# Performance work log

Hardware: AMD Instinct MI355X
Metric: run time of the kernel (lower is better)

The kernel has to match this reference:

```python
import jax, jax.numpy as jnp
import numpy as np

H = 16          # num heads
DH = 64         # head dim
D = H * DH      # hidden = 1024


def setup_inputs() -> dict:
    key = jax.random.key(0)
    ks = jax.random.split(key, 9)
    s = 1.0 / np.sqrt(D)
    return {
        "hidden_states": jax.random.normal(ks[0], (4, 2048, D), dtype=jnp.float32),
        "Wq": jax.random.normal(ks[1], (D, D), dtype=jnp.float32) * s,
        "bq": jax.random.normal(ks[2], (D,), dtype=jnp.float32) * 0.02,
        "Wk": jax.random.normal(ks[3], (D, D), dtype=jnp.float32) * s,
        "bk": jax.random.normal(ks[4], (D,), dtype=jnp.float32) * 0.02,
        "Wv": jax.random.normal(ks[5], (D, D), dtype=jnp.float32) * s,
        "bv": jax.random.normal(ks[6], (D,), dtype=jnp.float32) * 0.02,
        "Wo": jax.random.normal(ks[7], (D, D), dtype=jnp.float32) * s,
        "bo": jax.random.normal(ks[8], (D,), dtype=jnp.float32) * 0.02,
    }


def _split_heads(x):  # [B,S,D] -> [B,H,S,DH]
    B, S, _ = x.shape
    return x.reshape(B, S, H, DH).transpose(0, 2, 1, 3)


def reference(hidden_states, Wq, bq, Wk, bk, Wv, bv, Wo, bo):
    # torch Linear: y = x @ W.T + b  (W stored as [out, in])
    q = _split_heads(jnp.einsum('bsd,ed->bse', hidden_states, Wq) + bq)
    k = _split_heads(jnp.einsum('bsd,ed->bse', hidden_states, Wk) + bk)
    v = _split_heads(jnp.einsum('bsd,ed->bse', hidden_states, Wv) + bv)
    scores = jnp.einsum('bhqd,bhkd->bhqk', q, k) / np.sqrt(DH)
    probs = jax.nn.softmax(scores, axis=-1)  # fused softmax+matmul in original
    ctx = jnp.einsum('bhqk,bhkd->bhqd', probs, v)
    B, _, S, _ = ctx.shape
    ctx = ctx.transpose(0, 2, 1, 3).reshape(B, S, D)
    out = jnp.einsum('bsd,ed->bse', ctx, Wo) + bo
    return out  # weights are None (vis=False); dropout rate asserted 0
```

## Files before the change

### kernel.cpp

```cpp
#include <hip/hip_runtime.h>


typedef __bf16 bf16;
typedef __bf16 bf16x8 __attribute__((ext_vector_type(8)));
typedef __bf16 bf16x4 __attribute__((ext_vector_type(4)));
typedef float  floatx4 __attribute__((ext_vector_type(4)));

#define NB   4
#define SEQ  2048
#define NH   16
#define DH   64
#define DIM  1024
#define MTOT (NB * SEQ)

#define CEXP 0.18033688f

__device__ __forceinline__ floatx4 zero4() {
    floatx4 z; z[0] = 0.f; z[1] = 0.f; z[2] = 0.f; z[3] = 0.f; return z;
}

__device__ __forceinline__ void load_lds16(const bf16* g, bf16* l) {
    __builtin_amdgcn_global_load_lds(
        (__attribute__((address_space(1))) void*)g,
        (__attribute__((address_space(3))) void*)l,
        16, 0, 0);
}

__global__ __launch_bounds__(256) void cvt_all(const float* __restrict__ X,
                                               const float* __restrict__ w0,
                                               const float* __restrict__ w1,
                                               const float* __restrict__ w2,
                                               const float* __restrict__ w3,
                                               bf16* __restrict__ Xb,
                                               bf16* __restrict__ Wb) {
    const size_t MD = (size_t)MTOT * DIM;
    const size_t DD = (size_t)DIM * DIM;
    size_t i = ((size_t)blockIdx.x * 256 + threadIdx.x) * 4;
    float4 f; bf16* dst;
    if (i < MD) {
        f = *(const float4*)(X + i);
        dst = Xb + i;
    } else {
        size_t off = i - MD;
        int w = (int)(off >> 20);
        size_t wi = off & (DD - 1);
        const float* ws = (w == 0) ? w0 : (w == 1) ? w1 : (w == 2) ? w2 : w3;
        f = *(const float4*)(ws + wi);
        dst = Wb + off;
    }
    bf16x4 o;
    o[0] = (bf16)f.x; o[1] = (bf16)f.y; o[2] = (bf16)f.z; o[3] = (bf16)f.w;
    *(bf16x4*)dst = o;
}

#define QKV_TILE(T_, DO_STAGE_, WAITSTR_) do {                                 \
    const bf16* bA_ = smem + ((T_) & 3) * 16384;                               \
    const bf16* bB_ = bA_ + 8192;                                              \
    if (DO_STAGE_) {                                                           \
        bf16* sA_ = smem + (((T_) + 3) & 3) * 16384;                           \
        const int ko_ = ((T_) + 3) * 32;                                       \
        load_lds16(gA0 + ko_, sA_ + soff0);                                    \
        load_lds16(gA1 + ko_, sA_ + soff1);                                    \
        load_lds16(gB0 + ko_, sA_ + 8192 + soff0);                             \
        load_lds16(gB1 + ko_, sA_ + 8192 + soff1);                             \
    }                                                                          \
    bf16x8 afr_[4], bfg_[4];                                                   \
    _Pragma("unroll")                                                          \
    for (int mf = 0; mf < 4; mf++) afr_[mf] = *(const bf16x8*)(bA_ + aoff[mf]);\
    _Pragma("unroll")                                                          \
    for (int nf = 0; nf < 4; nf++) bfg_[nf] = *(const bf16x8*)(bB_ + boff[nf]);\
    __builtin_amdgcn_s_setprio(1);                                             \
    _Pragma("unroll")                                                          \
    for (int mf = 0; mf < 4; mf++)                                             \
        _Pragma("unroll")                                                      \
        for (int nf = 0; nf < 4; nf++)                                         \
            acc[mf][nf] = __builtin_amdgcn_mfma_f32_16x16x32_bf16(             \
                afr_[mf], bfg_[nf], acc[mf][nf], 0, 0, 0);                     \
    __builtin_amdgcn_s_setprio(0);                                             \
    _Pragma("unroll")                                                          \
    for (int mf = 0; mf < 4; mf++)                                             \
        afr_[mf] = *(const bf16x8*)(bA_ + aoff[4 + mf]);                       \
    __builtin_amdgcn_s_setprio(1);                                             \
    _Pragma("unroll")                                                          \
    for (int mf = 0; mf < 4; mf++)                                             \
        _Pragma("unroll")                                                      \
        for (int nf = 0; nf < 4; nf++)                                         \
            acc[4 + mf][nf] = __builtin_amdgcn_mfma_f32_16x16x32_bf16(         \
                afr_[mf], bfg_[nf], acc[4 + mf][nf], 0, 0, 0);                 \
    __builtin_amdgcn_s_setprio(0);                                             \
    asm volatile(WAITSTR_ ::: "memory");                                       \
    __builtin_amdgcn_s_barrier();                                              \
} while (0)

__global__ __launch_bounds__(512, 2) void gemm_qkv(const bf16* __restrict__ A,
                                                   const bf16* __restrict__ W,
                                                   const float* __restrict__ bq,
                                                   const float* __restrict__ bk,
                                                   const float* __restrict__ bv,
                                                   bf16* __restrict__ Qo,
                                                   bf16* __restrict__ Ko,
                                                   bf16* __restrict__ Vt) {
    __shared__ __align__(16) bf16 smem[4 * 16384];

    const int tid  = threadIdx.x;
    const int wave = tid >> 6, lane = tid & 63;
    const int quad = lane >> 4, l16 = lane & 15;
    const int wr = wave >> 2, wc = wave & 3;

    const int wg = (blockIdx.x & 7) * 48 + (blockIdx.x >> 3);
    const int mt = wg / 12, inner = wg % 12;
    const int sel = inner >> 2, nt = inner & 3;
    const int m0 = mt * 256, n0 = nt * 256;

    const bf16* Wsel = W + (size_t)(sel * DIM + n0) * DIM;
    const float* bias = (sel == 0) ? bq : (sel == 1) ? bk : bv;

    int aoff[8], boff[4];
#pragma unroll
    for (int mf = 0; mf < 8; mf++) {
        const int row = wr * 128 + mf * 16 + l16;
        aoff[mf] = row * 32 + ((quad ^ ((row >> 1) & 3)) * 8);
    }
#pragma unroll
    for (int nf = 0; nf < 4; nf++) {
        const int row = wc * 64 + nf * 16 + l16;
        boff[nf] = row * 32 + ((quad ^ ((row >> 1) & 3)) * 8);
    }

    const int c0 = tid, c1 = tid + 512;
    const int ra0 = c0 >> 2, qa0 = (c0 & 3) ^ ((ra0 >> 1) & 3);
    const int ra1 = c1 >> 2, qa1 = (c1 & 3) ^ ((ra1 >> 1) & 3);
    const bf16* gA0 = A + (size_t)(m0 + ra0) * DIM + qa0 * 8;
    const bf16* gA1 = A + (size_t)(m0 + ra1) * DIM + qa1 * 8;
    const bf16* gB0 = Wsel + (size_t)ra0 * DIM + qa0 * 8;
    const bf16* gB1 = Wsel + (size_t)ra1 * DIM + qa1 * 8;
    const int soff0 = (wave * 64) * 8;
    const int soff1 = (512 + wave * 64) * 8;

    floatx4 acc[8][4];
#pragma unroll
    for (int mf = 0; mf < 8; mf++)
#pragma unroll
        for (int nf = 0; nf < 4; nf++) acc[mf][nf] = zero4();

#pragma unroll
    for (int kt = 0; kt < 3; kt++) {
        bf16* sA = smem + kt * 16384;
        bf16* sB = sA + 8192;
        load_lds16(gA0 + kt * 32, sA + soff0);
        load_lds16(gA1 + kt * 32, sA + soff1);
        load_lds16(gB0 + kt * 32, sB + soff0);
        load_lds16(gB1 + kt * 32, sB + soff1);
    }
    asm volatile("s_waitcnt vmcnt(8)" ::: "memory");
    __builtin_amdgcn_s_barrier();

    const int NT = DIM / 32;
#pragma unroll 1
    for (int t = 0; t < NT - 3; t++)
        QKV_TILE(t, true, "s_waitcnt vmcnt(8)");
    QKV_TILE(NT - 3, false, "s_waitcnt vmcnt(4)");
    QKV_TILE(NT - 2, false, "s_waitcnt vmcnt(0)");
    QKV_TILE(NT - 1, false, "s_waitcnt vmcnt(0)");

    if (sel < 2) {
        bf16* C = (sel == 0) ? Qo : Ko;
        const float scale = (sel == 0) ? CEXP : 1.0f;
#pragma unroll
        for (int mf = 0; mf < 8; mf++) {
            const int rbase = m0 + wr * 128 + mf * 16 + quad * 4;
#pragma unroll
            for (int nf = 0; nf < 4; nf++) {
                const int col = n0 + wc * 64 + nf * 16 + l16;
                const float bval = bias[col];
#pragma unroll
                for (int i = 0; i < 4; i++)
                    C[(size_t)(rbase + i) * DIM + col] =
                        (bf16)((acc[mf][nf][i] + bval) * scale);
            }
        }
    } else {
        const int b  = m0 >> 11;
        const int s0 = m0 & (SEQ - 1);
#pragma unroll
        for (int mf = 0; mf < 8; mf++) {
            const int mb = wr * 128 + mf * 16 + quad * 4;
#pragma unroll
            for (int nf = 0; nf < 4; nf++) {
                const int n_loc = wc * 64 + nf * 16 + l16;
                const float bval = bias[n0 + n_loc];
                bf16x4 pk;
#pragma unroll
                for (int i = 0; i < 4; i++) pk[i] = (bf16)(acc[mf][nf][i] + bval);
                const int e = n_loc * 256 + (((mb * 2) ^ ((n_loc & 7) << 4)) >> 1);
                *(bf16x4*)(smem + e) = pk;
            }
        }
        asm volatile("s_waitcnt lgkmcnt(0)" ::: "memory");
        __builtin_amdgcn_s_barrier();
#pragma unroll
        for (int p = 0; p < 16; p++) {
            const int c = p * 512 + tid;
            const int n_loc = c >> 5, mc = (c & 31) * 8;
            const int e = n_loc * 256 + (((mc * 2) ^ ((n_loc & 7) << 4)) >> 1);
            bf16x8 v = *(const bf16x8*)(smem + e);
            const int dg = n0 + n_loc;
            const int hh = dg >> 6, d = dg & 63;
            bf16* op = Vt + ((size_t)(b * NH + hh) * DH + d) * SEQ + s0 + mc;
            *(bf16x8*)op = v;
        }
    }
}

__global__ __launch_bounds__(256) void gemm_out(const bf16* __restrict__ A,
                                                const bf16* __restrict__ W,
                                                const float* __restrict__ bias,
                                                float* __restrict__ C) {
    __shared__ __align__(16) bf16 As[128 * 32];
    __shared__ __align__(16) bf16 Bs[128 * 32];

    const int tid  = threadIdx.x;
    const int wave = tid >> 6, lane = tid & 63;
    const int quad = lane >> 4, l16 = lane & 15;
    const int m0 = blockIdx.y * 128, n0 = blockIdx.x * 128;
    const int wm = (wave & 1) * 64, wn = (wave >> 1) * 64;

    floatx4 acc[4][4];
#pragma unroll
    for (int mi = 0; mi < 4; mi++)
#pragma unroll
        for (int ni = 0; ni < 4; ni++) acc[mi][ni] = zero4();

    for (int k0 = 0; k0 < DIM; k0 += 32) {
        __syncthreads();
#pragma unroll
        for (int i = 0; i < 2; i++) {
            const int cb = wave * 128 + i * 64;
            const int c  = cb + lane;
            const int row = c >> 2;
            const int kc  = (c & 3) * 8;
            load_lds16(A + (size_t)(m0 + row) * DIM + k0 + kc, &As[cb * 8]);
            load_lds16(W + (size_t)(n0 + row) * DIM + k0 + kc, &Bs[cb * 8]);
        }
        __syncthreads();

        bf16x8 af[4], bfr[4];
#pragma unroll
        for (int mi = 0; mi < 4; mi++)
            af[mi] = *(const bf16x8*)&As[(wm + mi * 16 + l16) * 32 + quad * 8];
#pragma unroll
        for (int ni = 0; ni < 4; ni++)
            bfr[ni] = *(const bf16x8*)&Bs[(wn + ni * 16 + l16) * 32 + quad * 8];
#pragma unroll
        for (int mi = 0; mi < 4; mi++)
#pragma unroll
            for (int ni = 0; ni < 4; ni++)
                acc[mi][ni] = __builtin_amdgcn_mfma_f32_16x16x32_bf16(
                    af[mi], bfr[ni], acc[mi][ni], 0, 0, 0);
    }

#pragma unroll
    for (int mi = 0; mi < 4; mi++) {
        const int rbase = m0 + wm + mi * 16 + quad * 4;
#pragma unroll
        for (int ni = 0; ni < 4; ni++) {
            const int col = n0 + wn + ni * 16 + l16;
            const float bval = bias[col];
#pragma unroll
            for (int i = 0; i < 4; i++)
                C[(size_t)(rbase + i) * DIM + col] = acc[mi][ni][i] + bval;
        }
    }
}

__global__ __launch_bounds__(256, 2) void attn_kernel(const bf16* __restrict__ Q,
                                                      const bf16* __restrict__ K,
                                                      const bf16* __restrict__ Vt,
                                                      bf16* __restrict__ Ctx) {
    __shared__ __align__(16) bf16 Ks[2][64 * 64];
    __shared__ __align__(16) bf16 Vs[2][64 * 64];

    const int tid  = threadIdx.x;
    const int wave = tid >> 6, lane = tid & 63;
    const int quad = lane >> 4, l16 = lane & 15;
    const int xcd = blockIdx.x & 7;
    const int j   = blockIdx.x >> 3;
    const int bh  = xcd * 8 + (j >> 3);
    const int qb  = j & 7;
    const int b   = bh >> 4, h = bh & 15;

    const size_t base_bh = (size_t)b * SEQ * DIM + (size_t)h * DH;
    const size_t base_v  = (size_t)bh * DH * SEQ;
    const int qt = qb * 256 + wave * 64;

    bf16x8 aq[4][2];
#pragma unroll
    for (int m = 0; m < 4; m++) {
        const bf16* qp = Q + base_bh + (size_t)(qt + m * 16 + l16) * DIM + quad * 8;
        aq[m][0] = *(const bf16x8*)qp;
        aq[m][1] = *(const bf16x8*)(qp + 32);
    }

    const int sc = wave * 128 + lane;
    int srow[2], scol[2];
    srow[0] = sc >> 3;        srow[1] = (sc + 64) >> 3;
    scol[0] = (sc & 7) ^ (srow[0] & 7);
    scol[1] = ((sc + 64) & 7) ^ (srow[1] & 7);
    auto kvloc = [](int r) {
        const int w = r >> 5, rw = r & 31, r4 = rw & 15;
        return w * 32 + ((rw >> 4) << 2) + ((r4 >> 2) << 3) + (r4 & 3);
    };
    const bf16* kga = K + base_bh + (size_t)kvloc(srow[0]) * DIM + scol[0] * 8;
    const bf16* kgb = K + base_bh + (size_t)kvloc(srow[1]) * DIM + scol[1] * 8;
    const bf16* vga = Vt + base_v + (size_t)srow[0] * SEQ + scol[0] * 8;
    const bf16* vgb = Vt + base_v + (size_t)srow[1] * SEQ + scol[1] * 8;
    const int ldsa = (wave * 128) * 8, ldsb = (wave * 128 + 64) * 8;

    int koa[4], kob[4], vo[2][4];
#pragma unroll
    for (int g = 0; g < 4; g++) {
        const int krow = g * 16 + l16;
        koa[g] = (krow * 8 + (quad ^ (krow & 7))) * 8;
        kob[g] = (krow * 8 + ((4 + quad) ^ (krow & 7))) * 8;
    }
#pragma unroll
    for (int w = 0; w < 2; w++)
#pragma unroll
        for (int dt = 0; dt < 4; dt++) {
            const int d = dt * 16 + l16;
            vo[w][dt] = d * 64 + ((4 * w + quad) ^ (d & 7)) * 8;
        }

    bf16x8 ones8;
#pragma unroll
    for (int i = 0; i < 8; i++) ones8[i] = (bf16)1.0f;

    floatx4 acc[4][4], accl[4];
#pragma unroll
    for (int m = 0; m < 4; m++) {
        accl[m] = zero4();
#pragma unroll
        for (int dt = 0; dt < 4; dt++) acc[m][dt] = zero4();
    }

    load_lds16(kga, &Ks[0][ldsa]);
    load_lds16(kgb, &Ks[0][ldsb]);
    load_lds16(vga, &Vs[0][ldsa]);
    load_lds16(vgb, &Vs[0][ldsb]);

    for (int it = 0; it < SEQ / 64; it++) {
        __syncthreads();
        const int cur = it & 1;
        if (it + 1 < SEQ / 64) {
            const int nxt = cur ^ 1;
            const size_t kvn = (size_t)(it + 1) * 64;
            load_lds16(kga + kvn * DIM, &Ks[nxt][ldsa]);
            load_lds16(kgb + kvn * DIM, &Ks[nxt][ldsb]);
            load_lds16(vga + kvn, &Vs[nxt][ldsa]);
            load_lds16(vgb + kvn, &Vs[nxt][ldsb]);
        }

#pragma unroll
        for (int w = 0; w < 2; w++) {
            const bf16x8 ke0 = *(const bf16x8*)&Ks[cur][koa[2 * w]];
            const bf16x8 ke1 = *(const bf16x8*)&Ks[cur][kob[2 * w]];
            const bf16x8 ko0 = *(const bf16x8*)&Ks[cur][koa[2 * w + 1]];
            const bf16x8 ko1 = *(const bf16x8*)&Ks[cur][kob[2 * w + 1]];
            bf16x8 pw[4];
            __builtin_amdgcn_s_setprio(1);
#pragma unroll
            for (int m = 0; m < 4; m++) {
                floatx4 sa = zero4(), sb = zero4();
                sa = __builtin_amdgcn_mfma_f32_16x16x32_bf16(ke0, aq[m][0], sa, 0, 0, 0);
                sa = __builtin_amdgcn_mfma_f32_16x16x32_bf16(ke1, aq[m][1], sa, 0, 0, 0);
                sb = __builtin_amdgcn_mfma_f32_16x16x32_bf16(ko0, aq[m][0], sb, 0, 0, 0);
                sb = __builtin_amdgcn_mfma_f32_16x16x32_bf16(ko1, aq[m][1], sb, 0, 0, 0);
                bf16x8 p;
#pragma unroll
                for (int i = 0; i < 4; i++) {
                    p[i]     = (bf16)__builtin_amdgcn_exp2f(sa[i]);
                    p[4 + i] = (bf16)__builtin_amdgcn_exp2f(sb[i]);
                }
                pw[m] = p;
            }
            __builtin_amdgcn_s_setprio(0);
            bf16x8 vf[4];
#pragma unroll
            for (int dt = 0; dt < 4; dt++)
                vf[dt] = *(const bf16x8*)&Vs[cur][vo[w][dt]];
            __builtin_amdgcn_s_setprio(1);
#pragma unroll
            for (int m = 0; m < 4; m++) {
#pragma unroll
                for (int dt = 0; dt < 4; dt++)
                    acc[m][dt] = __builtin_amdgcn_mfma_f32_16x16x32_bf16(
                        pw[m], vf[dt], acc[m][dt], 0, 0, 0);
                accl[m] = __builtin_amdgcn_mfma_f32_16x16x32_bf16(
                    pw[m], ones8, accl[m], 0, 0, 0);
            }
            __builtin_amdgcn_s_setprio(0);
        }
    }

#pragma unroll
    for (int m = 0; m < 4; m++) {
        float inv[4];
#pragma unroll
        for (int i = 0; i < 4; i++) inv[i] = 1.0f / accl[m][i];
        bf16* cp = Ctx + base_bh + (size_t)(qt + m * 16 + quad * 4) * DIM + l16;
#pragma unroll
        for (int i = 0; i < 4; i++)
#pragma unroll
            for (int dt = 0; dt < 4; dt++)
                cp[(size_t)i * DIM + dt * 16] = (bf16)(acc[m][dt][i] * inv[i]);
    }
}

extern "C" void kernel_launch(void* const* d_in, const int* in_sizes, int n_in,
                              void* d_out, int out_size, void* d_ws, size_t ws_size,
                              hipStream_t stream) {
    const float* X  = (const float*)d_in[0];
    const float* Wq = (const float*)d_in[1];
    const float* bq = (const float*)d_in[2];
    const float* Wk = (const float*)d_in[3];
    const float* bk = (const float*)d_in[4];
    const float* Wv = (const float*)d_in[5];
    const float* bv = (const float*)d_in[6];
    const float* Wo = (const float*)d_in[7];
    const float* bo = (const float*)d_in[8];
    float* out = (float*)d_out;

    const size_t MD = (size_t)MTOT * DIM;
    const size_t DD = (size_t)DIM * DIM;

    bf16* Xb  = (bf16*)d_ws;
    bf16* Qb  = Xb + MD;
    bf16* Kb  = Qb + MD;
    bf16* Vtb = Kb + MD;
    bf16* Wqb = Vtb + MD;
    bf16* Wob = Wqb + 3 * DD;
    if (ws_size < (MD * 4 + DD * 4) * sizeof(bf16)) return;

    cvt_all<<<(int)((MD + 4 * DD) / 4 / 256), 256, 0, stream>>>(
        X, Wq, Wk, Wv, Wo, Xb, Wqb);

    gemm_qkv<<<384, 512, 0, stream>>>(Xb, Wqb, bq, bk, bv, Qb, Kb, Vtb);

    attn_kernel<<<NB * NH * (SEQ / 256), 256, 0, stream>>>(Qb, Kb, Vtb, Xb);

    gemm_out<<<dim3(8, MTOT / 128), 256, 0, stream>>>(Xb, Wob, bo, out);
}
```

Measured before the change: 260.6 us.

## Deepen attention K/V pipeline to four LDS stages with explicit vmcnt waits

Changes the attention kernel's K/V staging from a double buffer to a four-slot LDS ring that prefetches three tiles ahead. __syncthreads is replaced by explicit s_waitcnt vmcnt counts plus s_barrier. The inner loop is rewritten so the exp2 of one QK half overlaps the MFMAs of the other half and the PV MFMAs. The goal is to hide global-load latency and interleave VALU exp with matrix work. In exchange, LDS use doubles to 64KB per block, which may limit occupancy at two blocks per CU, and the hand-counted vmcnt values are fragile.

```diff
diff --git a/kernel.cpp b/kernel.cpp
--- a/kernel.cpp
+++ b/kernel.cpp
@@ -273,12 +273,104 @@
     }
 }
 
+#define ATTN_MFMA(A_, B_, C_) __builtin_amdgcn_mfma_f32_16x16x32_bf16(A_, B_, C_, 0, 0, 0)
+
+#define ATTN_TILE(T_, DO_STAGE_, DO_WAIT_, WAITSTR_) do {                      \
+    const int cur_ = (T_) & 3;                                                 \
+    if (DO_STAGE_) {                                                           \
+        const int nb_ = ((T_) + 3) & 3;                                        \
+        const size_t kvn_ = (size_t)((T_) + 3) * 64;                           \
+        load_lds16(kga + kvn_ * DIM, &Ks[nb_][ldsa]);                          \
+        load_lds16(kgb + kvn_ * DIM, &Ks[nb_][ldsb]);                          \
+        load_lds16(vga + kvn_, &Vs[nb_][ldsa]);                                \
+        load_lds16(vgb + kvn_, &Vs[nb_][ldsb]);                                \
+    }                                                                          \
+                                                      \
+    bf16x8 ke0_ = *(const bf16x8*)&Ks[cur_][koa[0]];                           \
+    bf16x8 ke1_ = *(const bf16x8*)&Ks[cur_][kob[0]];                           \
+    bf16x8 ko0_ = *(const bf16x8*)&Ks[cur_][koa[1]];                           \
+    bf16x8 ko1_ = *(const bf16x8*)&Ks[cur_][kob[1]];                           \
+    floatx4 sa0_[4], sb0_[4];                                                  \
+    _Pragma("unroll")                                                          \
+    for (int m = 0; m < 4; m++) {                                              \
+        floatx4 sa = zero4(), sb = zero4();                                    \
+        sa = ATTN_MFMA(ke0_, aq[m][0], sa);                                    \
+        sa = ATTN_MFMA(ke1_, aq[m][1], sa);                                    \
+        sb = ATTN_MFMA(ko0_, aq[m][0], sb);                                    \
+        sb = ATTN_MFMA(ko1_, aq[m][1], sb);                                    \
+        sa0_[m] = sa; sb0_[m] = sb;                                            \
+    }                                                                          \
+        \
+    bf16x8 kf1_[4];                                                            \
+    kf1_[0] = *(const bf16x8*)&Ks[cur_][koa[2]];                               \
+    kf1_[1] = *(const bf16x8*)&Ks[cur_][kob[2]];                               \
+    kf1_[2] = *(const bf16x8*)&Ks[cur_][koa[3]];                               \
+    kf1_[3] = *(const bf16x8*)&Ks[cur_][kob[3]];                               \
+    bf16x8 vf0_[4];                                                            \
+    _Pragma("unroll")                                                          \
+    for (int dt = 0; dt < 4; dt++)                                             \
+        vf0_[dt] = *(const bf16x8*)&Vs[cur_][vo[0][dt]];                       \
+               \
+    bf16x8 pw0_[4];                                                            \
+    _Pragma("unroll")                                                          \
+    for (int m = 0; m < 4; m++) {                                              \
+        bf16x8 p;                                                              \
+        _Pragma("unroll")                                                      \
+        for (int i = 0; i < 4; i++) {                                          \
+            p[i]     = (bf16)__builtin_amdgcn_exp2f(sa0_[m][i]);               \
+            p[4 + i] = (bf16)__builtin_amdgcn_exp2f(sb0_[m][i]);               \
+        }                                                                      \
+        pw0_[m] = p;                                                           \
+    }                                                                          \
+                                                                   \
+    floatx4 sa1_[4], sb1_[4];                                                  \
+    _Pragma("unroll")                                                          \
+    for (int m = 0; m < 4; m++) {                                              \
+        floatx4 sa = zero4(), sb = zero4();                                    \
+        sa = ATTN_MFMA(kf1_[0], aq[m][0], sa);                                 \
+        sa = ATTN_MFMA(kf1_[1], aq[m][1], sa);                                 \
+        sb = ATTN_MFMA(kf1_[2], aq[m][0], sb);                                 \
+        sb = ATTN_MFMA(kf1_[3], aq[m][1], sb);                                 \
+        sa1_[m] = sa; sb1_[m] = sb;                                            \
+    }                                                                          \
+                   \
+    bf16x8 vf1_[4];                                                            \
+    _Pragma("unroll")                                                          \
+    for (int dt = 0; dt < 4; dt++)                                             \
+        vf1_[dt] = *(const bf16x8*)&Vs[cur_][vo[1][dt]];                       \
+    bf16x8 pw1_[4];                                                            \
+    _Pragma("unroll")                                                          \
+    for (int m = 0; m < 4; m++) {                                              \
+        _Pragma("unroll")                                                      \
+        for (int dt = 0; dt < 4; dt++)                                         \
+            acc[m][dt] = ATTN_MFMA(pw0_[m], vf0_[dt], acc[m][dt]);             \
+        accl[m] = ATTN_MFMA(pw0_[m], ones8, accl[m]);                          \
+        bf16x8 p;                                                              \
+        _Pragma("unroll")                                                      \
+        for (int i = 0; i < 4; i++) {                                          \
+            p[i]     = (bf16)__builtin_amdgcn_exp2f(sa1_[m][i]);               \
+            p[4 + i] = (bf16)__builtin_amdgcn_exp2f(sb1_[m][i]);               \
+        }                                                                      \
+        pw1_[m] = p;                                                           \
+    }                                                                          \
+                                                                   \
+    _Pragma("unroll")                                                          \
+    for (int m = 0; m < 4; m++) {                                              \
+        _Pragma("unroll")                                                      \
+        for (int dt = 0; dt < 4; dt++)                                         \
+            acc[m][dt] = ATTN_MFMA(pw1_[m], vf1_[dt], acc[m][dt]);             \
+        accl[m] = ATTN_MFMA(pw1_[m], ones8, accl[m]);                          \
+    }                                                                          \
+    if (DO_WAIT_) asm volatile(WAITSTR_ ::: "memory");                         \
+    __builtin_amdgcn_s_barrier();                                              \
+} while (0)
+
 __global__ __launch_bounds__(256, 2) void attn_kernel(const bf16* __restrict__ Q,
                                                       const bf16* __restrict__ K,
                                                       const bf16* __restrict__ Vt,
                                                       bf16* __restrict__ Ctx) {
-    __shared__ __align__(16) bf16 Ks[2][64 * 64];
-    __shared__ __align__(16) bf16 Vs[2][64 * 64];
+    __shared__ __align__(16) bf16 Ks[4][64 * 64];
+    __shared__ __align__(16) bf16 Vs[4][64 * 64];
 
     const int tid  = threadIdx.x;
     const int wave = tid >> 6, lane = tid & 63;
@@ -343,64 +435,24 @@
         for (int dt = 0; dt < 4; dt++) acc[m][dt] = zero4();
     }
 
-    load_lds16(kga, &Ks[0][ldsa]);
-    load_lds16(kgb, &Ks[0][ldsb]);
-    load_lds16(vga, &Vs[0][ldsa]);
-    load_lds16(vgb, &Vs[0][ldsb]);
-
-    for (int it = 0; it < SEQ / 64; it++) {
-        __syncthreads();
-        const int cur = it & 1;
-        if (it + 1 < SEQ / 64) {
-            const int nxt = cur ^ 1;
-            const size_t kvn = (size_t)(it + 1) * 64;
-            load_lds16(kga + kvn * DIM, &Ks[nxt][ldsa]);
-            load_lds16(kgb + kvn * DIM, &Ks[nxt][ldsb]);
-            load_lds16(vga + kvn, &Vs[nxt][ldsa]);
-            load_lds16(vgb + kvn, &Vs[nxt][ldsb]);
-        }
-
-#pragma unroll
-        for (int w = 0; w < 2; w++) {
-            const bf16x8 ke0 = *(const bf16x8*)&Ks[cur][koa[2 * w]];
-            const bf16x8 ke1 = *(const bf16x8*)&Ks[cur][kob[2 * w]];
-            const bf16x8 ko0 = *(const bf16x8*)&Ks[cur][koa[2 * w + 1]];
-            const bf16x8 ko1 = *(const bf16x8*)&Ks[cur][kob[2 * w + 1]];
-            bf16x8 pw[4];
-            __builtin_amdgcn_s_setprio(1);
-#pragma unroll
-            for (int m = 0; m < 4; m++) {
-                floatx4 sa = zero4(), sb = zero4();
-                sa = __builtin_amdgcn_mfma_f32_16x16x32_bf16(ke0, aq[m][0], sa, 0, 0, 0);
-                sa = __builtin_amdgcn_mfma_f32_16x16x32_bf16(ke1, aq[m][1], sa, 0, 0, 0);
-                sb = __builtin_amdgcn_mfma_f32_16x16x32_bf16(ko0, aq[m][0], sb, 0, 0, 0);
-                sb = __builtin_amdgcn_mfma_f32_16x16x32_bf16(ko1, aq[m][1], sb, 0, 0, 0);
-                bf16x8 p;
-#pragma unroll
-                for (int i = 0; i < 4; i++) {
-                    p[i]     = (bf16)__builtin_amdgcn_exp2f(sa[i]);
-                    p[4 + i] = (bf16)__builtin_amdgcn_exp2f(sb[i]);
-                }
-                pw[m] = p;
-            }
-            __builtin_amdgcn_s_setprio(0);
-            bf16x8 vf[4];
-#pragma unroll
-            for (int dt = 0; dt < 4; dt++)
-                vf[dt] = *(const bf16x8*)&Vs[cur][vo[w][dt]];
-            __builtin_amdgcn_s_setprio(1);
-#pragma unroll
-            for (int m = 0; m < 4; m++) {
-#pragma unroll
-                for (int dt = 0; dt < 4; dt++)
-                    acc[m][dt] = __builtin_amdgcn_mfma_f32_16x16x32_bf16(
-                        pw[m], vf[dt], acc[m][dt], 0, 0, 0);
-                accl[m] = __builtin_amdgcn_mfma_f32_16x16x32_bf16(
-                    pw[m], ones8, accl[m], 0, 0, 0);
-            }
-            __builtin_amdgcn_s_setprio(0);
-        }
-    }
+#pragma unroll
+    for (int kt = 0; kt < 3; kt++) {
+        const size_t kvn = (size_t)kt * 64;
+        load_lds16(kga + kvn * DIM, &Ks[kt][ldsa]);
+        load_lds16(kgb + kvn * DIM, &Ks[kt][ldsb]);
+        load_lds16(vga + kvn, &Vs[kt][ldsa]);
+        load_lds16(vgb + kvn, &Vs[kt][ldsb]);
+    }
+    asm volatile("s_waitcnt vmcnt(8)" ::: "memory");
+    __builtin_amdgcn_s_barrier();
+
+    const int NT = SEQ / 64;
+#pragma unroll 1
+    for (int t = 0; t < NT - 3; t++)
+        ATTN_TILE(t, true, true, "s_waitcnt vmcnt(8)");
+    ATTN_TILE(NT - 3, false, true, "s_waitcnt vmcnt(4)");
+    ATTN_TILE(NT - 2, false, true, "s_waitcnt vmcnt(0)");
+    ATTN_TILE(NT - 1, false, false, "");
 
 #pragma unroll
     for (int m = 0; m < 4; m++) {
```

Result: no change. 257.6 us (-1.2%).
